# Kernel tuning notes

Hardware: AMD Instinct MI355X
Metric: run time of the kernel (lower is better)

Reference implementation:

```python
import jax, jax.numpy as jnp
import numpy as np

ENCODER_STRIDE = 320
TEMPERATURE = 1.0


def setup_inputs() -> dict:
    key = jax.random.key(0)
    k1, k2, k3, k4 = jax.random.split(key, 4)
    B, D, T, K = 8, 512, 4096, 4096
    student_features = jax.random.normal(k1, (B, D, T), dtype=jnp.float32)
    codebook = jax.random.normal(k2, (K, D), dtype=jnp.float32)
    teacher_codes = jax.random.randint(k3, (B, T), 0, K, dtype=jnp.int64)
    lengths = jax.random.randint(k4, (B,), 0, T * ENCODER_STRIDE, dtype=jnp.int64)
    return {
        "student_features": student_features,
        "codebook": codebook,
        "teacher_codes": teacher_codes,
        "lengths": lengths,
    }


def reference(student_features, codebook, teacher_codes, lengths):
    B, D, T = student_features.shape
    # length mask over frames: frame t is valid if its start sample < length
    frame_starts = jnp.arange(T, dtype=jnp.int64) * ENCODER_STRIDE  # [T]
    mask = (frame_starts[None, :] < lengths[:, None]).astype(student_features.dtype)  # [B,T]

    z = jnp.transpose(student_features, (0, 2, 1)).reshape(-1, D)  # [N,D], N=B*T

    # cdist p=2: sqrt(|z|^2 + |c|^2 - 2 z.c)
    z2 = jnp.sum(z * z, axis=1, keepdims=True)            # [N,1]
    c2 = jnp.sum(codebook * codebook, axis=1)[None, :]    # [1,K]
    d2 = z2 + c2 - 2.0 * (z @ codebook.T)                 # [N,K]
    dists = jnp.sqrt(jnp.maximum(d2, 1e-12))

    soft_weights = jax.nn.softmax(-dists / TEMPERATURE, axis=1)  # [N,K]
    soft_recon = soft_weights @ codebook                          # [N,D]

    codes_flat = teacher_codes.reshape(-1)                        # [N]
    target_embeddings = jax.lax.stop_gradient(codebook[codes_flat])  # [N,D]

    diff_sq = jnp.mean((soft_recon - target_embeddings) ** 2, axis=1).reshape(B, T)
    loss = jnp.sum(diff_sq * mask) / (jnp.sum(mask) + 1e-8)
    return loss
```

## Files before the change

kernel.cpp:

```cpp
#include <hip/hip_runtime.h>
#include <hip/hip_bf16.h>


#define BB 8
#define DD 512
#define TT 4096
#define KKK 4096
#define ENC_STRIDE 320
#define KT 32
#define NKT (KKK / KT)
#define NW 8
#define ROWS 128
#define KBROW 2056
#define KBBYTES 4112
#define BUFB (8 * KBBYTES)

#define WS_C2    256
#define WS_RTS   16640
#define WS_CBH   32768
#define WS_PART  4227072ULL
#define WS_ML    (WS_PART + 67108864ULL)
#define WS_NEED  (WS_ML + 524288ULL)

typedef __attribute__((ext_vector_type(8))) short bf16x8;
typedef __attribute__((ext_vector_type(4))) float f32x4;

union FragU { bf16x8 v; uint2 h2[2]; ushort us[8]; unsigned long long q[2]; uint4 u4; };

static __device__ __forceinline__ ushort f2bf(float x) {
  unsigned u = __float_as_uint(x);
  unsigned r = (u + 0x7FFFu + ((u >> 16) & 1u)) >> 16;
  return (ushort)r;
}
static __device__ __forceinline__ uint2 f4tobf(float4 v) {
  uint2 r;
  r.x = (unsigned)f2bf(v.x) | ((unsigned)f2bf(v.y) << 16);
  r.y = (unsigned)f2bf(v.z) | ((unsigned)f2bf(v.w) << 16);
  return r;
}
static __device__ __forceinline__ unsigned pk2bf(float lo, float hi) {
  return (__float_as_uint(lo) >> 16) | (__float_as_uint(hi) & 0xFFFF0000u);
}
static __device__ __forceinline__ float bfh2f(ushort h) {
  return __uint_as_float(((unsigned)h) << 16);
}
static __device__ __forceinline__ void gld_lds16(const void* g, void* l) {
  __builtin_amdgcn_global_load_lds(
      (const __attribute__((address_space(1))) unsigned*)g,
      (__attribute__((address_space(3))) unsigned*)l, 16, 0, 0);
}
static __device__ __forceinline__ unsigned lds_addr(const void* p) {
  return (unsigned)(size_t)(const __attribute__((address_space(3))) char*)p;
}

__global__ __launch_bounds__(256) void vq_prep(const float* __restrict__ cb,
                                               float* __restrict__ c2,
                                               ushort* __restrict__ cbh) {
  int k = blockIdx.x * 4 + (threadIdx.x >> 6);
  int lane = threadIdx.x & 63;
  const float4* p = (const float4*)(cb + (size_t)k * DD + lane * 8);
  float4 a = p[0], b = p[1];
  if (cbh) {
    uint2 pa = f4tobf(a), pb = f4tobf(b);
    *(uint4*)(cbh + (size_t)k * DD + lane * 8) = make_uint4(pa.x, pa.y, pb.x, pb.y);
  }
  float s = a.x*a.x + a.y*a.y + a.z*a.z + a.w*a.w
          + b.x*b.x + b.y*b.y + b.z*b.z + b.w*b.w;
  #pragma unroll
  for (int m = 1; m <= 32; m <<= 1) s += __shfl_xor(s, m);
  if (lane == 0) c2[k] = s;
}

__global__ void vq_plan(const int* __restrict__ lens, int* __restrict__ hdr,
                        int* __restrict__ rts) {
  int n = 0;
  for (int b2 = 0; b2 < BB; ++b2) {
    int v = (lens[b2] + (ENC_STRIDE - 1)) / ENC_STRIDE;
    v = v < TT ? v : TT;
    int tiles = (v + 127) >> 7;
    for (int t = 0; t < tiles; ++t) rts[n++] = (b2 << 5) | t;
  }
  hdr[0] = n;
  hdr[1] = (n * 128 + 255) >> 8;
  hdr[2] = n * 128;
}

__global__ __launch_bounds__(512, 2) void vq_main_ws(
    const float* __restrict__ sf,
    const ushort* __restrict__ cbh,
    const float* __restrict__ c2,
    const int* __restrict__ hdr,
    const int* __restrict__ rts,
    ushort* __restrict__ recon_p,
    float* __restrict__ ml) {
  __shared__ __align__(128) ushort cs[4][8][KBROW];
  __shared__ __align__(16) ushort wlds[2][NW][16][40];
  __shared__ float  alds[2][ROWS];
  __shared__ float  llds[ROWS];
  __shared__ int    flagv[128];

  const int Q = hdr[1], total = hdr[2];
  int start = blockIdx.x * Q;
  if (Q == 0 || start >= total) return;
  int end = start + Q;
  end = end < total ? end : total;
  int slot = blockIdx.x * 2;

  const int tid = threadIdx.x;
  const int w  = tid >> 6;
  const int l  = tid & 63;
  const int lg = l >> 4;
  const int ln = l & 15;
  const int sbase = (w * 4 + ((l >> 1) & 3)) * DD + (l >> 3) * 16 + (l & 1) * 8;
  const unsigned score_lane = (unsigned)((ln >> 2) * KBBYTES + (ln & 3) * 32
                                         + (lg >> 1) * 128 + (lg & 1) * 16);
  const unsigned tr_lane = (unsigned)(lg * KBBYTES + w * 512 + ln * 8);
  const unsigned cs0a = lds_addr(&cs[0][0][0]);

  while (start < end) {
    const int rt = start >> 7;
    const int k0 = start & 127;
    int seg_end = (rt + 1) << 7;
    seg_end = seg_end < end ? seg_end : end;
    const int klen = seg_end - start;
    const int rtv = rts[rt];
    const int b  = rtv >> 5;
    const int t0 = (rtv & 31) << 7;

    for (int i2 = tid; i2 < klen; i2 += 512) flagv[i2] = 0;

    const float* sfb = sf + (size_t)b * DD * TT;
    const int trow = t0 + w * 16 + ln;
    bf16x8 za[16];
    float z2 = 0.f;
    #pragma unroll
    for (int f = 0; f < 16; ++f) {
      #pragma unroll
      for (int j = 0; j < 8; ++j) {
        int d = f * 32 + lg * 8 + j;
        float v = __builtin_nontemporal_load(&sfb[(size_t)d * TT + trow]);
        z2 += v * v;
        za[f][j] = (short)f2bf(v);
      }
    }
    z2 += __shfl_xor(z2, 16);
    z2 += __shfl_xor(z2, 32);

    auto stage = [&](int kta, int buf) {
      const ushort* gb = cbh + (size_t)kta * KT * DD + sbase;
      ushort* lb = &cs[buf][w][0];
      #pragma unroll
      for (int q = 0; q < 4; ++q) gld_lds16(gb + q * 128, lb + q * 512);
    };

    stage(k0, 0);
    if (klen > 1) stage(k0 + 1, 1);
    if (klen > 2) stage(k0 + 2, 2);

    float mrow = -1e30f, lrow = 0.f;
    f32x4 acc[8][4];
    #pragma unroll
    for (int r = 0; r < 8; ++r)
      #pragma unroll
      for (int nt = 0; nt < 4; ++nt) acc[r][nt] = (f32x4){0.f, 0.f, 0.f, 0.f};

    f32x4 sc0, sc1;
    auto scores = [&](int sbuf) {
      const char* csb = (const char*)&cs[sbuf][0][0];
      f32x4 e0s = (f32x4){0,0,0,0}, o0s = (f32x4){0,0,0,0};
      f32x4 e1s = (f32x4){0,0,0,0}, o1s = (f32x4){0,0,0,0};
      __builtin_amdgcn_s_setprio(1);
      #pragma unroll
      for (int f = 0; f < 8; ++f) {
        bf16x8 ae0 = *(const bf16x8*)(csb + score_lane + (2 * f) * 256);
        bf16x8 ao0 = *(const bf16x8*)(csb + score_lane + (2 * f + 1) * 256);
        bf16x8 ae1 = *(const bf16x8*)(csb + score_lane + 16448 + (2 * f) * 256);
        bf16x8 ao1 = *(const bf16x8*)(csb + score_lane + 16448 + (2 * f + 1) * 256);
        e0s = __builtin_amdgcn_mfma_f32_16x16x32_bf16(ae0, za[2 * f],     e0s, 0, 0, 0);
        o0s = __builtin_amdgcn_mfma_f32_16x16x32_bf16(ao0, za[2 * f + 1], o0s, 0, 0, 0);
        e1s = __builtin_amdgcn_mfma_f32_16x16x32_bf16(ae1, za[2 * f],     e1s, 0, 0, 0);
        o1s = __builtin_amdgcn_mfma_f32_16x16x32_bf16(ao1, za[2 * f + 1], o1s, 0, 0, 0);
      }
      __builtin_amdgcn_s_setprio(0);
      sc0 = e0s + o0s;
      sc1 = e1s + o1s;
    };

    __syncthreads();
    scores(0);
    {
      const float4 c2a = *(const float4*)(c2 + k0 * KT + lg * 4);
      const float4 c2b = *(const float4*)(c2 + k0 * KT + 16 + lg * 4);
      float c2v[8] = {c2a.x, c2a.y, c2a.z, c2a.w, c2b.x, c2b.y, c2b.z, c2b.w};
      float sv[8];
      #pragma unroll
      for (int v = 0; v < 4; ++v) {
        sv[v]     = -sqrtf(fmaxf(z2 + c2v[v]     - 2.f * sc0[v], 1e-12f));
        sv[4 + v] = -sqrtf(fmaxf(z2 + c2v[4 + v] - 2.f * sc1[v], 1e-12f));
      }
      float lmax = sv[0];
      #pragma unroll
      for (int i = 1; i < 8; ++i) lmax = fmaxf(lmax, sv[i]);
      float tmax = fmaxf(lmax, __shfl_xor(lmax, 16));
      tmax = fmaxf(tmax, __shfl_xor(tmax, 32));
      float el[8], lsum = 0.f;
      #pragma unroll
      for (int i = 0; i < 8; ++i) { el[i] = __expf(sv[i] - lmax); lsum += el[i]; }
      mrow = tmax;
      float factor = __expf(lmax - tmax);
      float esum = lsum * factor;
      esum += __shfl_xor(esum, 16);
      esum += __shfl_xor(esum, 32);
      lrow = esum;
      uint4 pk;
      pk.x = pk2bf(el[0] * factor, el[1] * factor);
      pk.y = pk2bf(el[2] * factor, el[3] * factor);
      pk.z = pk2bf(el[4] * factor, el[5] * factor);
      pk.w = pk2bf(el[6] * factor, el[7] * factor);
      *(uint4*)&wlds[0][w][ln][lg * 8] = pk;
      if (lg == 0) alds[0][w * 16 + ln] = 1.f;
    }

    #pragma unroll 1
    for (int li = 1; li < klen; ++li) {
      __syncthreads();
      if (li + 2 < klen) stage(k0 + li + 2, (li + 2) & 3);

      scores(li & 3);

      const int kta = k0 + li;
      const float4 c2a = *(const float4*)(c2 + kta * KT + lg * 4);
      const float4 c2b = *(const float4*)(c2 + kta * KT + 16 + lg * 4);
      float c2v[8] = {c2a.x, c2a.y, c2a.z, c2a.w, c2b.x, c2b.y, c2b.z, c2b.w};
      float sv[8];
      #pragma unroll
      for (int v = 0; v < 4; ++v) {
        sv[v]     = -sqrtf(fmaxf(z2 + c2v[v]     - 2.f * sc0[v], 1e-12f));
        sv[4 + v] = -sqrtf(fmaxf(z2 + c2v[4 + v] - 2.f * sc1[v], 1e-12f));
      }
      float lmax = sv[0];
      #pragma unroll
      for (int i = 1; i < 8; ++i) lmax = fmaxf(lmax, sv[i]);
      float el[8], lsum = 0.f;
      #pragma unroll
      for (int i = 0; i < 8; ++i) { el[i] = __expf(sv[i] - lmax); lsum += el[i]; }

      const int lim1 = li - 1;
      const int s = lim1 & 1;
      const unsigned trb = cs0a + (unsigned)(lim1 & 3) * BUFB + tr_lane;
      unsigned long long tq0[4], tq1[4];
      #pragma unroll
      for (int nt = 0; nt < 4; ++nt) {
        asm volatile("ds_read_b64_tr_b16 %0, %2 offset:%3\n\t"
                     "ds_read_b64_tr_b16 %1, %2 offset:%4"
                     : "=&v"(tq0[nt]), "=&v"(tq1[nt])
                     : "v"(trb), "i"(nt * 128), "i"(16448 + nt * 128));
      }

      float tmax = fmaxf(lmax, __shfl_xor(lmax, 16));
      tmax = fmaxf(tmax, __shfl_xor(tmax, 32));
      const bool defer = (tmax <= mrow + 8.f);
      const float mnew = defer ? mrow : tmax;
      const float factor = __expf(lmax - mnew);
      float esum = lsum * factor;
      esum += __shfl_xor(esum, 16);
      esum += __shfl_xor(esum, 32);
      const float alpha = defer ? 1.f : __expf(mrow - mnew);
      lrow = lrow * alpha + esum;
      mrow = mnew;
      uint4 pk;
      pk.x = pk2bf(el[0] * factor, el[1] * factor);
      pk.y = pk2bf(el[2] * factor, el[3] * factor);
      pk.z = pk2bf(el[4] * factor, el[5] * factor);
      pk.w = pk2bf(el[6] * factor, el[7] * factor);
      const int s2 = li & 1;
      *(uint4*)&wlds[s2][w][ln][lg * 8] = pk;
      if (lg == 0) alds[s2][w * 16 + ln] = alpha;
      if (!__all(defer) && l == 0) flagv[li] = 1;

      const int flg = flagv[lim1];
      asm volatile("s_waitcnt lgkmcnt(0)" ::: "memory");
      __builtin_amdgcn_sched_barrier(0);

      if (flg) {
        #pragma unroll
        for (int r = 0; r < 8; ++r)
          #pragma unroll
          for (int v = 0; v < 4; ++v) {
            float av = alds[s][r * 16 + lg * 4 + v];
            #pragma unroll
            for (int nt = 0; nt < 4; ++nt) acc[r][nt][v] *= av;
          }
      }
      FragU cf[4];
      #pragma unroll
      for (int nt = 0; nt < 4; ++nt) { cf[nt].q[0] = tq0[nt]; cf[nt].q[1] = tq1[nt]; }

      __builtin_amdgcn_s_setprio(1);
      #pragma unroll
      for (int rh = 0; rh < 2; ++rh) {
        bf16x8 wa4[4];
        #pragma unroll
        for (int r4 = 0; r4 < 4; ++r4)
          wa4[r4] = *(const bf16x8*)&wlds[s][rh * 4 + r4][ln][lg * 8];
        #pragma unroll
        for (int r4 = 0; r4 < 4; ++r4)
          #pragma unroll
          for (int nt = 0; nt < 4; ++nt)
            acc[rh * 4 + r4][nt] = __builtin_amdgcn_mfma_f32_16x16x32_bf16(
                wa4[r4], cf[nt].v, acc[rh * 4 + r4][nt], 0, 0, 0);
      }
      __builtin_amdgcn_s_setprio(0);
    }

    __syncthreads();
    {
      const int lim1 = klen - 1;
      const int s = lim1 & 1;
      const unsigned trb = cs0a + (unsigned)(lim1 & 3) * BUFB + tr_lane;
      unsigned long long tq0[4], tq1[4];
      #pragma unroll
      for (int nt = 0; nt < 4; ++nt) {
        asm volatile("ds_read_b64_tr_b16 %0, %2 offset:%3\n\t"
                     "ds_read_b64_tr_b16 %1, %2 offset:%4"
                     : "=&v"(tq0[nt]), "=&v"(tq1[nt])
                     : "v"(trb), "i"(nt * 128), "i"(16448 + nt * 128));
      }
      const int flg = flagv[lim1];
      asm volatile("s_waitcnt lgkmcnt(0)" ::: "memory");
      __builtin_amdgcn_sched_barrier(0);
      if (flg) {
        #pragma unroll
        for (int r = 0; r < 8; ++r)
          #pragma unroll
          for (int v = 0; v < 4; ++v) {
            float av = alds[s][r * 16 + lg * 4 + v];
            #pragma unroll
            for (int nt = 0; nt < 4; ++nt) acc[r][nt][v] *= av;
          }
      }
      FragU cf[4];
      #pragma unroll
      for (int nt = 0; nt < 4; ++nt) { cf[nt].q[0] = tq0[nt]; cf[nt].q[1] = tq1[nt]; }
      #pragma unroll
      for (int rh = 0; rh < 2; ++rh) {
        bf16x8 wa4[4];
        #pragma unroll
        for (int r4 = 0; r4 < 4; ++r4)
          wa4[r4] = *(const bf16x8*)&wlds[s][rh * 4 + r4][ln][lg * 8];
        #pragma unroll
        for (int r4 = 0; r4 < 4; ++r4)
          #pragma unroll
          for (int nt = 0; nt < 4; ++nt)
            acc[rh * 4 + r4][nt] = __builtin_amdgcn_mfma_f32_16x16x32_bf16(
                wa4[r4], cf[nt].v, acc[rh * 4 + r4][nt], 0, 0, 0);
      }
    }

    if (lg == 0) {
      llds[w * 16 + ln] = lrow;
      float2 mlv; mlv.x = mrow; mlv.y = lrow;
      *(float2*)&ml[(size_t)(slot * 128 + w * 16 + ln) * 2] = mlv;
    }
    __syncthreads();
    {
      ushort* rp = recon_p + (size_t)slot * (128 * 512);
      #pragma unroll
      for (int r = 0; r < 8; ++r) {
        #pragma unroll
        for (int v = 0; v < 4; ++v) {
          const int row = r * 16 + lg * 4 + v;
          const float lv = llds[row];
          #pragma unroll
          for (int nt = 0; nt < 4; ++nt) {
            const int d = w * 64 + nt * 16 + ln;
            rp[row * 512 + d] = f2bf(acc[r][nt][v] / lv);
          }
        }
      }
    }
    __syncthreads();

    start += klen;
    slot++;
  }
}

__global__ __launch_bounds__(512) void vq_merge(
    const ushort* __restrict__ recon_p, const float* __restrict__ ml,
    const int* __restrict__ hdr, const int* __restrict__ rts,
    const int* __restrict__ lens, const float* __restrict__ cb,
    const int* __restrict__ codes, float* __restrict__ num) {
  __shared__ float red[128];
  const int i = blockIdx.x;
  const int nact = hdr[0];
  if (i >= nact) return;
  const int Q = hdr[1], total = hdr[2];
  const int rtv = rts[i];
  const int b = rtv >> 5;
  const int t0 = (rtv & 31) << 7;
  int vcount = (lens[b] + (ENC_STRIDE - 1)) / ENC_STRIDE;
  vcount = vcount < TT ? vcount : TT;

  const int tid = threadIdx.x;
  const int r = tid >> 2;
  const int q = tid & 3;
  const int flat0 = i << 7, flat1 = flat0 + 128;
  int c_lo = flat0 / Q;
  int c_hi = (flat1 - 1) / Q;
  c_hi = c_hi < 255 ? c_hi : 255;

  float M = -1e30f;
  for (int c = c_lo; c <= c_hi; ++c) {
    const int cs_ = c * Q;
    int ce = cs_ + Q; ce = ce < total ? ce : total;
    if (cs_ >= flat1 || ce <= flat0) continue;
    const int slot = c * 2 + (i - (cs_ >> 7));
    M = fmaxf(M, ml[(size_t)(slot * 128 + r) * 2]);
  }
  float L = 0.f;
  for (int c = c_lo; c <= c_hi; ++c) {
    const int cs_ = c * Q;
    int ce = cs_ + Q; ce = ce < total ? ce : total;
    if (cs_ >= flat1 || ce <= flat0) continue;
    const int slot = c * 2 + (i - (cs_ >> 7));
    const float m_ = ml[(size_t)(slot * 128 + r) * 2];
    const float l_ = ml[(size_t)(slot * 128 + r) * 2 + 1];
    L += l_ * __expf(m_ - M);
  }
  const float invL = 1.f / L;

  const int tc = codes[b * TT + t0 + r];
  const float* targ = cb + (size_t)tc * DD + q * 128;

  float psum = 0.f;
  #pragma unroll 1
  for (int ch = 0; ch < 16; ++ch) {
    const int d0 = q * 128 + ch * 8;
    float rec[8] = {0.f, 0.f, 0.f, 0.f, 0.f, 0.f, 0.f, 0.f};
    for (int c = c_lo; c <= c_hi; ++c) {
      const int cs_ = c * Q;
      int ce = cs_ + Q; ce = ce < total ? ce : total;
      if (cs_ >= flat1 || ce <= flat0) continue;
      const int slot = c * 2 + (i - (cs_ >> 7));
      const float m_ = ml[(size_t)(slot * 128 + r) * 2];
      const float l_ = ml[(size_t)(slot * 128 + r) * 2 + 1];
      const float wn = l_ * __expf(m_ - M) * invL;
      const ushort* rp = recon_p + (size_t)slot * (128 * 512) + r * 512 + d0;
      FragU u; u.u4 = *(const uint4*)rp;
      #pragma unroll
      for (int j = 0; j < 8; ++j) rec[j] += wn * bfh2f(u.us[j]);
    }
    const float4 tg0 = *(const float4*)(targ + ch * 8);
    const float4 tg1 = *(const float4*)(targ + ch * 8 + 4);
    float tg[8] = {tg0.x, tg0.y, tg0.z, tg0.w, tg1.x, tg1.y, tg1.z, tg1.w};
    #pragma unroll
    for (int j = 0; j < 8; ++j) { float df = rec[j] - tg[j]; psum += df * df; }
  }
  psum += __shfl_xor(psum, 1);
  psum += __shfl_xor(psum, 2);
  if (q == 0) red[r] = ((t0 + r) < vcount) ? psum * (1.f / DD) : 0.f;
  __syncthreads();
  if (tid < 128) {
    float val = red[tid];
    val += __shfl_xor(val, 1);
    val += __shfl_xor(val, 2);
    val += __shfl_xor(val, 4);
    val += __shfl_xor(val, 8);
    val += __shfl_xor(val, 16);
    val += __shfl_xor(val, 32);
    if ((tid & 63) == 0) atomicAdd(num, val);
  }
}

template <int GLD>
__global__ __launch_bounds__(512, 2) void vq_main(
    const float* __restrict__ sf, const float* __restrict__ cb,
    const ushort* __restrict__ cbh, const int* __restrict__ codes,
    const int* __restrict__ lens, const float* __restrict__ c2,
    float* __restrict__ num) {
  __shared__ __align__(128) ushort cs[4][8][KBROW];
  __shared__ __align__(16) ushort wlds[2][NW][16][40];
  __shared__ float  alds[2][ROWS];
  __shared__ float  llds[ROWS];
  __shared__ float  diffred[ROWS];
  __shared__ int    flagv[NKT];

  const int bid = blockIdx.x;
  const int b  = bid >> 5;
  const int t0 = (bid & 31) << 7;
  const int len = lens[b];
  int vcount = (len + (ENC_STRIDE - 1)) / ENC_STRIDE;
  vcount = vcount < TT ? vcount : TT;
  if (t0 >= vcount) return;

  const int tid = threadIdx.x;
  const int w  = tid >> 6;
  const int l  = tid & 63;
  const int lg = l >> 4;
  const int ln = l & 15;

  for (int i = tid; i < ROWS; i += 512) diffred[i] = 0.f;
  for (int i = tid; i < NKT; i += 512) flagv[i] = 0;

  const float* sfb = sf + (size_t)b * DD * TT;
  const int trow = t0 + w * 16 + ln;
  bf16x8 za[16];
  float z2 = 0.f;
  #pragma unroll
  for (int f = 0; f < 16; ++f) {
    #pragma unroll
    for (int j = 0; j < 8; ++j) {
      int d = f * 32 + lg * 8 + j;
      float v = __builtin_nontemporal_load(&sfb[(size_t)d * TT + trow]);
      z2 += v * v;
      za[f][j] = (short)f2bf(v);
    }
  }
  z2 += __shfl_xor(z2, 16);
  z2 += __shfl_xor(z2, 32);

  const int sbase = (w * 4 + ((l >> 1) & 3)) * DD + (l >> 3) * 16 + (l & 1) * 8;
  auto stage = [&](int kt, int buf) {
    if (GLD) {
      const ushort* gb = cbh + (size_t)kt * KT * DD + sbase;
      ushort* lb = &cs[buf][w][0];
      #pragma unroll
      for (int q = 0; q < 4; ++q) gld_lds16(gb + q * 128, lb + q * 512);
    } else {
      const float* gb = cb + (size_t)kt * KT * DD + sbase;
      #pragma unroll
      for (int q = 0; q < 4; ++q) {
        float4 v0 = *(const float4*)(gb + q * 128);
        float4 v1 = *(const float4*)(gb + q * 128 + 4);
        uint2 a0 = f4tobf(v0), a1 = f4tobf(v1);
        *(uint4*)&cs[buf][w][q * 512 + l * 8] = make_uint4(a0.x, a0.y, a1.x, a1.y);
      }
    }
  };

  stage(0, 0); stage(1, 1); stage(2, 2);

  float mrow = -1e30f, lrow = 0.f;
  f32x4 acc[8][4];
  #pragma unroll
  for (int r = 0; r < 8; ++r)
    #pragma unroll
    for (int nt = 0; nt < 4; ++nt) acc[r][nt] = (f32x4){0.f, 0.f, 0.f, 0.f};

  const unsigned score_lane = (unsigned)((ln >> 2) * KBBYTES + (ln & 3) * 32
                                         + (lg >> 1) * 128 + (lg & 1) * 16);
  const unsigned tr_lane = (unsigned)(lg * KBBYTES + w * 512 + ln * 8);
  const unsigned cs0a = lds_addr(&cs[0][0][0]);

  f32x4 sc0, sc1;
  auto scores = [&](int sbuf) {
    const char* csb = (const char*)&cs[sbuf][0][0];
    f32x4 e0s = (f32x4){0,0,0,0}, o0s = (f32x4){0,0,0,0};
    f32x4 e1s = (f32x4){0,0,0,0}, o1s = (f32x4){0,0,0,0};
    __builtin_amdgcn_s_setprio(1);
    #pragma unroll
    for (int f = 0; f < 8; ++f) {
      bf16x8 ae0 = *(const bf16x8*)(csb + score_lane + (2 * f) * 256);
      bf16x8 ao0 = *(const bf16x8*)(csb + score_lane + (2 * f + 1) * 256);
      bf16x8 ae1 = *(const bf16x8*)(csb + score_lane + 16448 + (2 * f) * 256);
      bf16x8 ao1 = *(const bf16x8*)(csb + score_lane + 16448 + (2 * f + 1) * 256);
      e0s = __builtin_amdgcn_mfma_f32_16x16x32_bf16(ae0, za[2 * f],     e0s, 0, 0, 0);
      o0s = __builtin_amdgcn_mfma_f32_16x16x32_bf16(ao0, za[2 * f + 1], o0s, 0, 0, 0);
      e1s = __builtin_amdgcn_mfma_f32_16x16x32_bf16(ae1, za[2 * f],     e1s, 0, 0, 0);
      o1s = __builtin_amdgcn_mfma_f32_16x16x32_bf16(ao1, za[2 * f + 1], o1s, 0, 0, 0);
    }
    __builtin_amdgcn_s_setprio(0);
    sc0 = e0s + o0s;
    sc1 = e1s + o1s;
  };

  __syncthreads();
  scores(0);
  {
    const float4 c2a = *(const float4*)(c2 + lg * 4);
    const float4 c2b = *(const float4*)(c2 + 16 + lg * 4);
    float c2v[8] = {c2a.x, c2a.y, c2a.z, c2a.w, c2b.x, c2b.y, c2b.z, c2b.w};
    float sv[8];
    #pragma unroll
    for (int v = 0; v < 4; ++v) {
      sv[v]     = -sqrtf(fmaxf(z2 + c2v[v]     - 2.f * sc0[v], 1e-12f));
      sv[4 + v] = -sqrtf(fmaxf(z2 + c2v[4 + v] - 2.f * sc1[v], 1e-12f));
    }
    float lmax = sv[0];
    #pragma unroll
    for (int i = 1; i < 8; ++i) lmax = fmaxf(lmax, sv[i]);
    float tmax = fmaxf(lmax, __shfl_xor(lmax, 16));
    tmax = fmaxf(tmax, __shfl_xor(tmax, 32));
    float el[8], lsum = 0.f;
    #pragma unroll
    for (int i = 0; i < 8; ++i) { el[i] = __expf(sv[i] - lmax); lsum += el[i]; }
    mrow = tmax;
    float factor = __expf(lmax - tmax);
    float esum = lsum * factor;
    esum += __shfl_xor(esum, 16);
    esum += __shfl_xor(esum, 32);
    lrow = esum;
    uint4 pk;
    pk.x = pk2bf(el[0] * factor, el[1] * factor);
    pk.y = pk2bf(el[2] * factor, el[3] * factor);
    pk.z = pk2bf(el[4] * factor, el[5] * factor);
    pk.w = pk2bf(el[6] * factor, el[7] * factor);
    *(uint4*)&wlds[0][w][ln][lg * 8] = pk;
    if (lg == 0) alds[0][w * 16 + ln] = 1.f;
  }

  #pragma unroll 1
  for (int it = 1; it < NKT; ++it) {
    __syncthreads();
    if (it + 2 < NKT) stage(it + 2, (it + 2) & 3);
    scores(it & 3);

    const float4 c2a = *(const float4*)(c2 + it * KT + lg * 4);
    const float4 c2b = *(const float4*)(c2 + it * KT + 16 + lg * 4);
    float c2v[8] = {c2a.x, c2a.y, c2a.z, c2a.w, c2b.x, c2b.y, c2b.z, c2b.w};
    float sv[8];
    #pragma unroll
    for (int v = 0; v < 4; ++v) {
      sv[v]     = -sqrtf(fmaxf(z2 + c2v[v]     - 2.f * sc0[v], 1e-12f));
      sv[4 + v] = -sqrtf(fmaxf(z2 + c2v[4 + v] - 2.f * sc1[v], 1e-12f));
    }
    float lmax = sv[0];
    #pragma unroll
    for (int i = 1; i < 8; ++i) lmax = fmaxf(lmax, sv[i]);
    float el[8], lsum = 0.f;
    #pragma unroll
    for (int i = 0; i < 8; ++i) { el[i] = __expf(sv[i] - lmax); lsum += el[i]; }

    const int itm1 = it - 1;
    const int s = itm1 & 1;
    const unsigned trb = cs0a + (unsigned)(itm1 & 3) * BUFB + tr_lane;
    unsigned long long tq0[4], tq1[4];
    #pragma unroll
    for (int nt = 0; nt < 4; ++nt) {
      asm volatile("ds_read_b64_tr_b16 %0, %2 offset:%3\n\t"
                   "ds_read_b64_tr_b16 %1, %2 offset:%4"
                   : "=&v"(tq0[nt]), "=&v"(tq1[nt])
                   : "v"(trb), "i"(nt * 128), "i"(16448 + nt * 128));
    }

    float tmax = fmaxf(lmax, __shfl_xor(lmax, 16));
    tmax = fmaxf(tmax, __shfl_xor(tmax, 32));
    const bool defer = (tmax <= mrow + 8.f);
    const float mnew = defer ? mrow : tmax;
    const float factor = __expf(lmax - mnew);
    float esum = lsum * factor;
    esum += __shfl_xor(esum, 16);
    esum += __shfl_xor(esum, 32);
    const float alpha = defer ? 1.f : __expf(mrow - mnew);
    lrow = lrow * alpha + esum;
    mrow = mnew;
    uint4 pk;
    pk.x = pk2bf(el[0] * factor, el[1] * factor);
    pk.y = pk2bf(el[2] * factor, el[3] * factor);
    pk.z = pk2bf(el[4] * factor, el[5] * factor);
    pk.w = pk2bf(el[6] * factor, el[7] * factor);
    const int s2 = it & 1;
    *(uint4*)&wlds[s2][w][ln][lg * 8] = pk;
    if (lg == 0) alds[s2][w * 16 + ln] = alpha;
    if (!__all(defer) && l == 0) flagv[it] = 1;

    const int flg = flagv[itm1];
    asm volatile("s_waitcnt lgkmcnt(0)" ::: "memory");
    __builtin_amdgcn_sched_barrier(0);

    if (flg) {
      #pragma unroll
      for (int r = 0; r < 8; ++r)
        #pragma unroll
        for (int v = 0; v < 4; ++v) {
          float av = alds[s][r * 16 + lg * 4 + v];
          #pragma unroll
          for (int nt = 0; nt < 4; ++nt) acc[r][nt][v] *= av;
        }
    }
    FragU cf[4];
    #pragma unroll
    for (int nt = 0; nt < 4; ++nt) { cf[nt].q[0] = tq0[nt]; cf[nt].q[1] = tq1[nt]; }

    __builtin_amdgcn_s_setprio(1);
    #pragma unroll
    for (int rh = 0; rh < 2; ++rh) {
      bf16x8 wa4[4];
      #pragma unroll
      for (int r4 = 0; r4 < 4; ++r4)
        wa4[r4] = *(const bf16x8*)&wlds[s][rh * 4 + r4][ln][lg * 8];
      #pragma unroll
      for (int r4 = 0; r4 < 4; ++r4)
        #pragma unroll
        for (int nt = 0; nt < 4; ++nt)
          acc[rh * 4 + r4][nt] = __builtin_amdgcn_mfma_f32_16x16x32_bf16(
              wa4[r4], cf[nt].v, acc[rh * 4 + r4][nt], 0, 0, 0);
    }
    __builtin_amdgcn_s_setprio(0);
  }

  __syncthreads();
  {
    const int itm1 = NKT - 1;
    const int s = itm1 & 1;
    const unsigned trb = cs0a + (unsigned)(itm1 & 3) * BUFB + tr_lane;
    unsigned long long tq0[4], tq1[4];
    #pragma unroll
    for (int nt = 0; nt < 4; ++nt) {
      asm volatile("ds_read_b64_tr_b16 %0, %2 offset:%3\n\t"
                   "ds_read_b64_tr_b16 %1, %2 offset:%4"
                   : "=&v"(tq0[nt]), "=&v"(tq1[nt])
                   : "v"(trb), "i"(nt * 128), "i"(16448 + nt * 128));
    }
    const int flg = flagv[itm1];
    asm volatile("s_waitcnt lgkmcnt(0)" ::: "memory");
    __builtin_amdgcn_sched_barrier(0);
    if (flg) {
      #pragma unroll
      for (int r = 0; r < 8; ++r)
        #pragma unroll
        for (int v = 0; v < 4; ++v) {
          float av = alds[s][r * 16 + lg * 4 + v];
          #pragma unroll
          for (int nt = 0; nt < 4; ++nt) acc[r][nt][v] *= av;
        }
    }
    FragU cf[4];
    #pragma unroll
    for (int nt = 0; nt < 4; ++nt) { cf[nt].q[0] = tq0[nt]; cf[nt].q[1] = tq1[nt]; }
    #pragma unroll
    for (int rh = 0; rh < 2; ++rh) {
      bf16x8 wa4[4];
      #pragma unroll
      for (int r4 = 0; r4 < 4; ++r4)
        wa4[r4] = *(const bf16x8*)&wlds[s][rh * 4 + r4][ln][lg * 8];
      #pragma unroll
      for (int r4 = 0; r4 < 4; ++r4)
        #pragma unroll
        for (int nt = 0; nt < 4; ++nt)
          acc[rh * 4 + r4][nt] = __builtin_amdgcn_mfma_f32_16x16x32_bf16(
              wa4[r4], cf[nt].v, acc[rh * 4 + r4][nt], 0, 0, 0);
    }
  }

  if (lg == 0) llds[w * 16 + ln] = lrow;
  __syncthreads();
  const int* tcodes = codes + b * TT + t0;
  #pragma unroll
  for (int r = 0; r < 8; ++r) {
    float pv[4];
    #pragma unroll
    for (int v = 0; v < 4; ++v) {
      const int row = r * 16 + lg * 4 + v;
      const float lv = llds[row];
      const int tc = tcodes[row];
      const float* erow = cb + (size_t)tc * DD + w * 64;
      float ps = 0.f;
      #pragma unroll
      for (int nt = 0; nt < 4; ++nt) {
        float rc = acc[r][nt][v] / lv;
        float df = rc - erow[nt * 16 + ln];
        ps += df * df;
      }
      pv[v] = ps;
    }
    #pragma unroll
    for (int v = 0; v < 4; ++v) {
      pv[v] += __shfl_xor(pv[v], 1);
      pv[v] += __shfl_xor(pv[v], 2);
      pv[v] += __shfl_xor(pv[v], 4);
      pv[v] += __shfl_xor(pv[v], 8);
    }
    if (ln == 0) {
      #pragma unroll
      for (int v = 0; v < 4; ++v)
        atomicAdd(&diffred[r * 16 + lg * 4 + v], pv[v]);
    }
  }
  __syncthreads();
  if (tid < ROWS) {
    float val = (t0 + tid < vcount) ? diffred[tid] * (1.f / DD) : 0.f;
    val += __shfl_xor(val, 1);
    val += __shfl_xor(val, 2);
    val += __shfl_xor(val, 4);
    val += __shfl_xor(val, 8);
    val += __shfl_xor(val, 16);
    val += __shfl_xor(val, 32);
    if ((tid & 63) == 0) atomicAdd(num, val);
  }
}

__global__ void vq_finalize(const float* __restrict__ num,
                            const int* __restrict__ lens,
                            float* __restrict__ out) {
  float denom = 0.f;
  for (int b = 0; b < BB; ++b) {
    int v = (lens[b] + (ENC_STRIDE - 1)) / ENC_STRIDE;
    v = v < TT ? v : TT;
    denom += (float)v;
  }
  out[0] = num[0] / (denom + 1e-8f);
}

extern "C" void kernel_launch(void* const* d_in, const int* in_sizes, int n_in,
                              void* d_out, int out_size, void* d_ws, size_t ws_size,
                              hipStream_t stream) {
  const float* sf    = (const float*)d_in[0];
  const float* cb    = (const float*)d_in[1];
  const int*   codes = (const int*)d_in[2];
  const int*   lens  = (const int*)d_in[3];
  float* out = (float*)d_out;
  float* num = (float*)d_ws;
  int*   hdr = (int*)((char*)d_ws + 16);
  float* c2  = (float*)((char*)d_ws + WS_C2);
  int*   rts = (int*)((char*)d_ws + WS_RTS);
  const size_t need_gld = WS_CBH + (size_t)KKK * DD * sizeof(ushort);
  ushort* cbh = (ws_size >= need_gld) ? (ushort*)((char*)d_ws + WS_CBH) : nullptr;

  (void)hipMemsetAsync(d_ws, 0, 4, stream);
  vq_prep<<<KKK / 4, 256, 0, stream>>>(cb, c2, cbh);

  if (cbh && ws_size >= WS_NEED) {
    ushort* recon_p = (ushort*)((char*)d_ws + WS_PART);
    float*  mlp     = (float*)((char*)d_ws + WS_ML);
    vq_plan<<<1, 1, 0, stream>>>(lens, hdr, rts);
    vq_main_ws<<<256, 512, 0, stream>>>(sf, cbh, c2, hdr, rts, recon_p, mlp);
    vq_merge<<<256, 512, 0, stream>>>(recon_p, mlp, hdr, rts, lens, cb, codes, num);
  } else {
    const int grid = (BB * TT) / ROWS;
    if (cbh)
      vq_main<1><<<grid, 512, 0, stream>>>(sf, cb, cbh, codes, lens, c2, num);
    else
      vq_main<0><<<grid, 512, 0, stream>>>(sf, cb, cbh, codes, lens, c2, num);
  }
  vq_finalize<<<1, 1, 0, stream>>>(num, lens, out);
}
```

Baseline: 390.3 us.

## Stagger wave phases so half the waves run recon before scores, plus merge split

Splits the main loop so waves 0-3 run scores then softmax then reconstruction, while waves 4-7 run reconstruction first. The aim is to spread the MFMA-heavy and VALU-heavy phases across waves so the units overlap instead of all waves contending for the same unit at once. It also replaces sqrtf with a raw v_sqrt_f32 instruction, which may slightly change precision. The merge kernel now uses a 2D grid with 8 threads per row and 64 rows per block to raise parallelism.

```diff
diff --git a/kernel.cpp b/kernel.cpp
--- a/kernel.cpp
+++ b/kernel.cpp
@@ -43,6 +43,9 @@
 }
 static __device__ __forceinline__ float bfh2f(ushort h) {
   return __uint_as_float(((unsigned)h) << 16);
+}
+static __device__ __forceinline__ float fsqrtf(float x) {
+  float r; asm("v_sqrt_f32 %0, %1" : "=v"(r) : "v"(x)); return r;
 }
 static __device__ __forceinline__ void gld_lds16(const void* g, void* l) {
   __builtin_amdgcn_global_load_lds(
@@ -186,17 +189,15 @@
       sc1 = e1s + o1s;
     };
 
-    __syncthreads();
-    scores(0);
-    {
-      const float4 c2a = *(const float4*)(c2 + k0 * KT + lg * 4);
-      const float4 c2b = *(const float4*)(c2 + k0 * KT + 16 + lg * 4);
+    auto softmax_full = [&](int kta, int li) {
+      const float4 c2a = *(const float4*)(c2 + kta * KT + lg * 4);
+      const float4 c2b = *(const float4*)(c2 + kta * KT + 16 + lg * 4);
       float c2v[8] = {c2a.x, c2a.y, c2a.z, c2a.w, c2b.x, c2b.y, c2b.z, c2b.w};
       float sv[8];
       #pragma unroll
       for (int v = 0; v < 4; ++v) {
-        sv[v]     = -sqrtf(fmaxf(z2 + c2v[v]     - 2.f * sc0[v], 1e-12f));
-        sv[4 + v] = -sqrtf(fmaxf(z2 + c2v[4 + v] - 2.f * sc1[v], 1e-12f));
+        sv[v]     = -fsqrtf(fmaxf(z2 + c2v[v]     - 2.f * sc0[v], 1e-12f));
+        sv[4 + v] = -fsqrtf(fmaxf(z2 + c2v[4 + v] - 2.f * sc1[v], 1e-12f));
       }
       float lmax = sv[0];
       #pragma unroll
@@ -206,66 +207,13 @@
       float el[8], lsum = 0.f;
       #pragma unroll
       for (int i = 0; i < 8; ++i) { el[i] = __expf(sv[i] - lmax); lsum += el[i]; }
-      mrow = tmax;
-      float factor = __expf(lmax - tmax);
-      float esum = lsum * factor;
-      esum += __shfl_xor(esum, 16);
-      esum += __shfl_xor(esum, 32);
-      lrow = esum;
-      uint4 pk;
-      pk.x = pk2bf(el[0] * factor, el[1] * factor);
-      pk.y = pk2bf(el[2] * factor, el[3] * factor);
-      pk.z = pk2bf(el[4] * factor, el[5] * factor);
-      pk.w = pk2bf(el[6] * factor, el[7] * factor);
-      *(uint4*)&wlds[0][w][ln][lg * 8] = pk;
-      if (lg == 0) alds[0][w * 16 + ln] = 1.f;
-    }
-
-    #pragma unroll 1
-    for (int li = 1; li < klen; ++li) {
-      __syncthreads();
-      if (li + 2 < klen) stage(k0 + li + 2, (li + 2) & 3);
-
-      scores(li & 3);
-
-      const int kta = k0 + li;
-      const float4 c2a = *(const float4*)(c2 + kta * KT + lg * 4);
-      const float4 c2b = *(const float4*)(c2 + kta * KT + 16 + lg * 4);
-      float c2v[8] = {c2a.x, c2a.y, c2a.z, c2a.w, c2b.x, c2b.y, c2b.z, c2b.w};
-      float sv[8];
-      #pragma unroll
-      for (int v = 0; v < 4; ++v) {
-        sv[v]     = -sqrtf(fmaxf(z2 + c2v[v]     - 2.f * sc0[v], 1e-12f));
-        sv[4 + v] = -sqrtf(fmaxf(z2 + c2v[4 + v] - 2.f * sc1[v], 1e-12f));
-      }
-      float lmax = sv[0];
-      #pragma unroll
-      for (int i = 1; i < 8; ++i) lmax = fmaxf(lmax, sv[i]);
-      float el[8], lsum = 0.f;
-      #pragma unroll
-      for (int i = 0; i < 8; ++i) { el[i] = __expf(sv[i] - lmax); lsum += el[i]; }
-
-      const int lim1 = li - 1;
-      const int s = lim1 & 1;
-      const unsigned trb = cs0a + (unsigned)(lim1 & 3) * BUFB + tr_lane;
-      unsigned long long tq0[4], tq1[4];
-      #pragma unroll
-      for (int nt = 0; nt < 4; ++nt) {
-        asm volatile("ds_read_b64_tr_b16 %0, %2 offset:%3\n\t"
-                     "ds_read_b64_tr_b16 %1, %2 offset:%4"
-                     : "=&v"(tq0[nt]), "=&v"(tq1[nt])
-                     : "v"(trb), "i"(nt * 128), "i"(16448 + nt * 128));
-      }
-
-      float tmax = fmaxf(lmax, __shfl_xor(lmax, 16));
-      tmax = fmaxf(tmax, __shfl_xor(tmax, 32));
-      const bool defer = (tmax <= mrow + 8.f);
-      const float mnew = defer ? mrow : tmax;
+      const bool defer = (li > 0) && (tmax <= mrow + 8.f);
+      const float mnew = defer ? mrow : fmaxf(tmax, mrow);
       const float factor = __expf(lmax - mnew);
       float esum = lsum * factor;
       esum += __shfl_xor(esum, 16);
       esum += __shfl_xor(esum, 32);
-      const float alpha = defer ? 1.f : __expf(mrow - mnew);
+      const float alpha = (li > 0 && !defer) ? __expf(mrow - mnew) : 1.f;
       lrow = lrow * alpha + esum;
       mrow = mnew;
       uint4 pk;
@@ -273,49 +221,12 @@
       pk.y = pk2bf(el[2] * factor, el[3] * factor);
       pk.z = pk2bf(el[4] * factor, el[5] * factor);
       pk.w = pk2bf(el[6] * factor, el[7] * factor);
-      const int s2 = li & 1;
-      *(uint4*)&wlds[s2][w][ln][lg * 8] = pk;
-      if (lg == 0) alds[s2][w * 16 + ln] = alpha;
-      if (!__all(defer) && l == 0) flagv[li] = 1;
-
-      const int flg = flagv[lim1];
-      asm volatile("s_waitcnt lgkmcnt(0)" ::: "memory");
-      __builtin_amdgcn_sched_barrier(0);
-
-      if (flg) {
-        #pragma unroll
-        for (int r = 0; r < 8; ++r)
-          #pragma unroll
-          for (int v = 0; v < 4; ++v) {
-            float av = alds[s][r * 16 + lg * 4 + v];
-            #pragma unroll
-            for (int nt = 0; nt < 4; ++nt) acc[r][nt][v] *= av;
-          }
-      }
-      FragU cf[4];
-      #pragma unroll
-      for (int nt = 0; nt < 4; ++nt) { cf[nt].q[0] = tq0[nt]; cf[nt].q[1] = tq1[nt]; }
-
-      __builtin_amdgcn_s_setprio(1);
-      #pragma unroll
-      for (int rh = 0; rh < 2; ++rh) {
-        bf16x8 wa4[4];
-        #pragma unroll
-        for (int r4 = 0; r4 < 4; ++r4)
-          wa4[r4] = *(const bf16x8*)&wlds[s][rh * 4 + r4][ln][lg * 8];
-        #pragma unroll
-        for (int r4 = 0; r4 < 4; ++r4)
-          #pragma unroll
-          for (int nt = 0; nt < 4; ++nt)
-            acc[rh * 4 + r4][nt] = __builtin_amdgcn_mfma_f32_16x16x32_bf16(
-                wa4[r4], cf[nt].v, acc[rh * 4 + r4][nt], 0, 0, 0);
-      }
-      __builtin_amdgcn_s_setprio(0);
-    }
-
-    __syncthreads();
-    {
-      const int lim1 = klen - 1;
+      *(uint4*)&wlds[li & 1][w][ln][lg * 8] = pk;
+      if (lg == 0) alds[li & 1][w * 16 + ln] = alpha;
+      if (li > 0 && !__all(defer) && l == 0) flagv[li] = 1;
+    };
+
+    auto recon_full = [&](int lim1) {
       const int s = lim1 & 1;
       const unsigned trb = cs0a + (unsigned)(lim1 & 3) * BUFB + tr_lane;
       unsigned long long tq0[4], tq1[4];
@@ -342,6 +253,7 @@
       FragU cf[4];
       #pragma unroll
       for (int nt = 0; nt < 4; ++nt) { cf[nt].q[0] = tq0[nt]; cf[nt].q[1] = tq1[nt]; }
+      __builtin_amdgcn_s_setprio(1);
       #pragma unroll
       for (int rh = 0; rh < 2; ++rh) {
         bf16x8 wa4[4];
@@ -355,7 +267,35 @@
             acc[rh * 4 + r4][nt] = __builtin_amdgcn_mfma_f32_16x16x32_bf16(
                 wa4[r4], cf[nt].v, acc[rh * 4 + r4][nt], 0, 0, 0);
       }
-    }
+      __builtin_amdgcn_s_setprio(0);
+    };
+
+    __syncthreads();
+    scores(0);
+    softmax_full(k0, 0);
+
+    if (w < 4) {
+      #pragma unroll 1
+      for (int li = 1; li < klen; ++li) {
+        __syncthreads();
+        if (li + 2 < klen) stage(k0 + li + 2, (li + 2) & 3);
+        scores(li & 3);
+        softmax_full(k0 + li, li);
+        recon_full(li - 1);
+      }
+    } else {
+      #pragma unroll 1
+      for (int li = 1; li < klen; ++li) {
+        __syncthreads();
+        if (li + 2 < klen) stage(k0 + li + 2, (li + 2) & 3);
+        recon_full(li - 1);
+        scores(li & 3);
+        softmax_full(k0 + li, li);
+      }
+    }
+
+    __syncthreads();
+    recon_full(klen - 1);
 
     if (lg == 0) {
       llds[w * 16 + ln] = lrow;
@@ -391,7 +331,7 @@
     const int* __restrict__ hdr, const int* __restrict__ rts,
     const int* __restrict__ lens, const float* __restrict__ cb,
     const int* __restrict__ codes, float* __restrict__ num) {
-  __shared__ float red[128];
+  __shared__ float red[64];
   const int i = blockIdx.x;
   const int nact = hdr[0];
   if (i >= nact) return;
@@ -403,8 +343,9 @@
   vcount = vcount < TT ? vcount : TT;
 
   const int tid = threadIdx.x;
-  const int r = tid >> 2;
-  const int q = tid & 3;
+  const int rl = tid >> 3;
+  const int q  = tid & 7;
+  const int r  = blockIdx.y * 64 + rl;
   const int flat0 = i << 7, flat1 = flat0 + 128;
   int c_lo = flat0 / Q;
   int c_hi = (flat1 - 1) / Q;
@@ -431,12 +372,12 @@
   const float invL = 1.f / L;
 
   const int tc = codes[b * TT + t0 + r];
-  const float* targ = cb + (size_t)tc * DD + q * 128;
+  const float* targ = cb + (size_t)tc * DD;
 
   float psum = 0.f;
   #pragma unroll 1
-  for (int ch = 0; ch < 16; ++ch) {
-    const int d0 = q * 128 + ch * 8;
+  for (int ch = 0; ch < 8; ++ch) {
+    const int d0 = q * 64 + ch * 8;
     float rec[8] = {0.f, 0.f, 0.f, 0.f, 0.f, 0.f, 0.f, 0.f};
     for (int c = c_lo; c <= c_hi; ++c) {
       const int cs_ = c * Q;
@@ -451,17 +392,18 @@
       #pragma unroll
       for (int j = 0; j < 8; ++j) rec[j] += wn * bfh2f(u.us[j]);
     }
-    const float4 tg0 = *(const float4*)(targ + ch * 8);
-    const float4 tg1 = *(const float4*)(targ + ch * 8 + 4);
+    const float4 tg0 = *(const float4*)(targ + d0);
+    const float4 tg1 = *(const float4*)(targ + d0 + 4);
     float tg[8] = {tg0.x, tg0.y, tg0.z, tg0.w, tg1.x, tg1.y, tg1.z, tg1.w};
     #pragma unroll
     for (int j = 0; j < 8; ++j) { float df = rec[j] - tg[j]; psum += df * df; }
   }
   psum += __shfl_xor(psum, 1);
   psum += __shfl_xor(psum, 2);
-  if (q == 0) red[r] = ((t0 + r) < vcount) ? psum * (1.f / DD) : 0.f;
+  psum += __shfl_xor(psum, 4);
+  if (q == 0) red[rl] = ((t0 + r) < vcount) ? psum * (1.f / DD) : 0.f;
   __syncthreads();
-  if (tid < 128) {
+  if (tid < 64) {
     float val = red[tid];
     val += __shfl_xor(val, 1);
     val += __shfl_xor(val, 2);
@@ -469,7 +411,7 @@
     val += __shfl_xor(val, 8);
     val += __shfl_xor(val, 16);
     val += __shfl_xor(val, 32);
-    if ((tid & 63) == 0) atomicAdd(num, val);
+    if (tid == 0) atomicAdd(num, val);
   }
 }
 
@@ -575,17 +517,15 @@
     sc1 = e1s + o1s;
   };
 
-  __syncthreads();
-  scores(0);
-  {
-    const float4 c2a = *(const float4*)(c2 + lg * 4);
-    const float4 c2b = *(const float4*)(c2 + 16 + lg * 4);
+  auto softmax_full = [&](int kta, int li) {
+    const float4 c2a = *(const float4*)(c2 + kta * KT + lg * 4);
+    const float4 c2b = *(const float4*)(c2 + kta * KT + 16 + lg * 4);
     float c2v[8] = {c2a.x, c2a.y, c2a.z, c2a.w, c2b.x, c2b.y, c2b.z, c2b.w};
     float sv[8];
     #pragma unroll
     for (int v = 0; v < 4; ++v) {
-      sv[v]     = -sqrtf(fmaxf(z2 + c2v[v]     - 2.f * sc0[v], 1e-12f));
-      sv[4 + v] = -sqrtf(fmaxf(z2 + c2v[4 + v] - 2.f * sc1[v], 1e-12f));
+      sv[v]     = -fsqrtf(fmaxf(z2 + c2v[v]     - 2.f * sc0[v], 1e-12f));
+      sv[4 + v] = -fsqrtf(fmaxf(z2 + c2v[4 + v] - 2.f * sc1[v], 1e-12f));
     }
     float lmax = sv[0];
     #pragma unroll
@@ -595,64 +535,13 @@
     float el[8], lsum = 0.f;
     #pragma unroll
     for (int i = 0; i < 8; ++i) { el[i] = __expf(sv[i] - lmax); lsum += el[i]; }
-    mrow = tmax;
-    float factor = __expf(lmax - tmax);
-    float esum = lsum * factor;
-    esum += __shfl_xor(esum, 16);
-    esum += __shfl_xor(esum, 32);
-    lrow = esum;
-    uint4 pk;
-    pk.x = pk2bf(el[0] * factor, el[1] * factor);
-    pk.y = pk2bf(el[2] * factor, el[3] * factor);
-    pk.z = pk2bf(el[4] * factor, el[5] * factor);
-    pk.w = pk2bf(el[6] * factor, el[7] * factor);
-    *(uint4*)&wlds[0][w][ln][lg * 8] = pk;
-    if (lg == 0) alds[0][w * 16 + ln] = 1.f;
-  }
-
-  #pragma unroll 1
-  for (int it = 1; it < NKT; ++it) {
-    __syncthreads();
-    if (it + 2 < NKT) stage(it + 2, (it + 2) & 3);
-    scores(it & 3);
-
-    const float4 c2a = *(const float4*)(c2 + it * KT + lg * 4);
-    const float4 c2b = *(const float4*)(c2 + it * KT + 16 + lg * 4);
-    float c2v[8] = {c2a.x, c2a.y, c2a.z, c2a.w, c2b.x, c2b.y, c2b.z, c2b.w};
-    float sv[8];
-    #pragma unroll
-    for (int v = 0; v < 4; ++v) {
-      sv[v]     = -sqrtf(fmaxf(z2 + c2v[v]     - 2.f * sc0[v], 1e-12f));
-      sv[4 + v] = -sqrtf(fmaxf(z2 + c2v[4 + v] - 2.f * sc1[v], 1e-12f));
-    }
-    float lmax = sv[0];
-    #pragma unroll
-    for (int i = 1; i < 8; ++i) lmax = fmaxf(lmax, sv[i]);
-    float el[8], lsum = 0.f;
-    #pragma unroll
-    for (int i = 0; i < 8; ++i) { el[i] = __expf(sv[i] - lmax); lsum += el[i]; }
-
-    const int itm1 = it - 1;
-    const int s = itm1 & 1;
-    const unsigned trb = cs0a + (unsigned)(itm1 & 3) * BUFB + tr_lane;
-    unsigned long long tq0[4], tq1[4];
-    #pragma unroll
-    for (int nt = 0; nt < 4; ++nt) {
-      asm volatile("ds_read_b64_tr_b16 %0, %2 offset:%3\n\t"
-                   "ds_read_b64_tr_b16 %1, %2 offset:%4"
-                   : "=&v"(tq0[nt]), "=&v"(tq1[nt])
-                   : "v"(trb), "i"(nt * 128), "i"(16448 + nt * 128));
-    }
-
-    float tmax = fmaxf(lmax, __shfl_xor(lmax, 16));
-    tmax = fmaxf(tmax, __shfl_xor(tmax, 32));
-    const bool defer = (tmax <= mrow + 8.f);
-    const float mnew = defer ? mrow : tmax;
+    const bool defer = (li > 0) && (tmax <= mrow + 8.f);
+    const float mnew = defer ? mrow : fmaxf(tmax, mrow);
     const float factor = __expf(lmax - mnew);
     float esum = lsum * factor;
     esum += __shfl_xor(esum, 16);
     esum += __shfl_xor(esum, 32);
-    const float alpha = defer ? 1.f : __expf(mrow - mnew);
+    const float alpha = (li > 0 && !defer) ? __expf(mrow - mnew) : 1.f;
     lrow = lrow * alpha + esum;
     mrow = mnew;
     uint4 pk;
@@ -660,15 +549,25 @@
     pk.y = pk2bf(el[2] * factor, el[3] * factor);
     pk.z = pk2bf(el[4] * factor, el[5] * factor);
     pk.w = pk2bf(el[6] * factor, el[7] * factor);
-    const int s2 = it & 1;
-    *(uint4*)&wlds[s2][w][ln][lg * 8] = pk;
-    if (lg == 0) alds[s2][w * 16 + ln] = alpha;
-    if (!__all(defer) && l == 0) flagv[it] = 1;
-
-    const int flg = flagv[itm1];
+    *(uint4*)&wlds[li & 1][w][ln][lg * 8] = pk;
+    if (lg == 0) alds[li & 1][w * 16 + ln] = alpha;
+    if (li > 0 && !__all(defer) && l == 0) flagv[li] = 1;
+  };
+
+  auto recon_full = [&](int lim1) {
+    const int s = lim1 & 1;
+    const unsigned trb = cs0a + (unsigned)(lim1 & 3) * BUFB + tr_lane;
+    unsigned long long tq0[4], tq1[4];
+    #pragma unroll
+    for (int nt = 0; nt < 4; ++nt) {
+      asm volatile("ds_read_b64_tr_b16 %0, %2 offset:%3\n\t"
+                   "ds_read_b64_tr_b16 %1, %2 offset:%4"
+                   : "=&v"(tq0[nt]), "=&v"(tq1[nt])
+                   : "v"(trb), "i"(nt * 128), "i"(16448 + nt * 128));
+    }
+    const int flg = flagv[lim1];
     asm volatile("s_waitcnt lgkmcnt(0)" ::: "memory");
     __builtin_amdgcn_sched_barrier(0);
-
     if (flg) {
       #pragma unroll
       for (int r = 0; r < 8; ++r)
@@ -682,7 +581,6 @@
     FragU cf[4];
     #pragma unroll
     for (int nt = 0; nt < 4; ++nt) { cf[nt].q[0] = tq0[nt]; cf[nt].q[1] = tq1[nt]; }
-
     __builtin_amdgcn_s_setprio(1);
     #pragma unroll
     for (int rh = 0; rh < 2; ++rh) {
@@ -698,51 +596,34 @@
               wa4[r4], cf[nt].v, acc[rh * 4 + r4][nt], 0, 0, 0);
     }
     __builtin_amdgcn_s_setprio(0);
-  }
+  };
 
   __syncthreads();
-  {
-    const int itm1 = NKT - 1;
-    const int s = itm1 & 1;
-    const unsigned trb = cs0a + (unsigned)(itm1 & 3) * BUFB + tr_lane;
-    unsigned long long tq0[4], tq1[4];
-    #pragma unroll
-    for (int nt = 0; nt < 4; ++nt) {
-      asm volatile("ds_read_b64_tr_b16 %0, %2 offset:%3\n\t"
-                   "ds_read_b64_tr_b16 %1, %2 offset:%4"
-                   : "=&v"(tq0[nt]), "=&v"(tq1[nt])
-                   : "v"(trb), "i"(nt * 128), "i"(16448 + nt * 128));
-    }
-    const int flg = flagv[itm1];
-    asm volatile("s_waitcnt lgkmcnt(0)" ::: "memory");
-    __builtin_amdgcn_sched_barrier(0);
-    if (flg) {
-      #pragma unroll
-      for (int r = 0; r < 8; ++r)
-        #pragma unroll
-        for (int v = 0; v < 4; ++v) {
-          float av = alds[s][r * 16 + lg * 4 + v];
-          #pragma unroll
-          for (int nt = 0; nt < 4; ++nt) acc[r][nt][v] *= av;
-        }
-    }
-    FragU cf[4];
-    #pragma unroll
-    for (int nt = 0; nt < 4; ++nt) { cf[nt].q[0] = tq0[nt]; cf[nt].q[1] = tq1[nt]; }
-    #pragma unroll
-    for (int rh = 0; rh < 2; ++rh) {
-      bf16x8 wa4[4];
-      #pragma unroll
-      for (int r4 = 0; r4 < 4; ++r4)
-        wa4[r4] = *(const bf16x8*)&wlds[s][rh * 4 + r4][ln][lg * 8];
-      #pragma unroll
-      for (int r4 = 0; r4 < 4; ++r4)
-        #pragma unroll
-        for (int nt = 0; nt < 4; ++nt)
-          acc[rh * 4 + r4][nt] = __builtin_amdgcn_mfma_f32_16x16x32_bf16(
-              wa4[r4], cf[nt].v, acc[rh * 4 + r4][nt], 0, 0, 0);
-    }
-  }
+  scores(0);
+  softmax_full(0, 0);
+
+  if (w < 4) {
+    #pragma unroll 1
+    for (int it = 1; it < NKT; ++it) {
+      __syncthreads();
+      if (it + 2 < NKT) stage(it + 2, (it + 2) & 3);
+      scores(it & 3);
+      softmax_full(it, it);
+      recon_full(it - 1);
+    }
+  } else {
+    #pragma unroll 1
+    for (int it = 1; it < NKT; ++it) {
+      __syncthreads();
+      if (it + 2 < NKT) stage(it + 2, (it + 2) & 3);
+      recon_full(it - 1);
+      scores(it & 3);
+      softmax_full(it, it);
+    }
+  }
+
+  __syncthreads();
+  recon_full(NKT - 1);
 
   if (lg == 0) llds[w * 16 + ln] = lrow;
   __syncthreads();
@@ -826,7 +707,7 @@
     float*  mlp     = (float*)((char*)d_ws + WS_ML);
     vq_plan<<<1, 1, 0, stream>>>(lens, hdr, rts);
     vq_main_ws<<<256, 512, 0, stream>>>(sf, cbh, c2, hdr, rts, recon_p, mlp);
-    vq_merge<<<256, 512, 0, stream>>>(recon_p, mlp, hdr, rts, lens, cb, codes, num);
+    vq_merge<<<dim3(256, 2), 512, 0, stream>>>(recon_p, mlp, hdr, rts, lens, cb, codes, num);
   } else {
     const int grid = (BB * TT) / ROWS;
     if (cbh)
```

Result: faster. 375.7 us (-3.7%).
